# Optimization experiments

Hardware: AMD Instinct MI355X
Metric: run time of the kernel (lower is better)

Reference implementation:

```python
import jax, jax.numpy as jnp
import numpy as np

N_A = N_B = N_C = 50000
E = 800000
D_IN = 256
D_OUT = 128
T_ATT = 64


def _spmm(row, col, val, ft, n_dst):
    # sparse [n_dst, n_src] @ ft : gather src rows, scale, scatter-add to dst
    return jax.ops.segment_sum(val[:, None] * ft[col], row, num_segments=n_dst)


def setup_inputs() -> dict:
    key = jax.random.key(0)
    ks = jax.random.split(key, 40)
    f32 = jnp.float32
    inp = {
        'x_a': jax.random.normal(ks[0], (N_A, D_IN), f32),
        'x_b': jax.random.normal(ks[1], (N_B, D_IN), f32),
        'x_c': jax.random.normal(ks[2], (N_C, D_IN), f32),
    }
    # COO adjacency per relation: (dst_row, src_col, value)
    rel = {'ab': (N_A, N_B), 'ac': (N_A, N_C), 'ba': (N_B, N_A), 'ca': (N_C, N_A)}
    i = 3
    for name, (nd, ns) in rel.items():
        inp['row_' + name] = jax.random.randint(ks[i], (E,), 0, nd); i += 1
        inp['col_' + name] = jax.random.randint(ks[i], (E,), 0, ns); i += 1
        inp['val_' + name] = jax.random.uniform(ks[i], (E,), f32); i += 1
    # learned parameters (xavier-ish scale)
    def w(k, shape, s=0.05):
        return jax.random.normal(k, shape, f32) * s
    inp['w_self_a'] = w(ks[i], (D_IN, D_OUT)); i += 1
    inp['w_self_b'] = w(ks[i], (D_IN, D_OUT)); i += 1
    inp['w_self_c'] = w(ks[i], (D_IN, D_OUT)); i += 1
    inp['W_ab'] = w(ks[i], (D_IN, D_OUT)); i += 1
    inp['W_ac'] = w(ks[i], (D_IN, D_OUT)); i += 1
    inp['W_ba'] = w(ks[i], (D_IN, D_OUT)); i += 1
    inp['W_ca'] = w(ks[i], (D_IN, D_OUT)); i += 1
    inp['bias_a'] = w(ks[i], (1, D_OUT)); i += 1
    inp['bias_b'] = w(ks[i], (1, D_OUT)); i += 1
    inp['bias_c'] = w(ks[i], (1, D_OUT)); i += 1
    inp['w_cat_a'] = w(ks[i], (2 * D_OUT, D_OUT)); i += 1
    inp['w_cat_b'] = w(ks[i], (2 * D_OUT, D_OUT)); i += 1
    inp['w_cat_c'] = w(ks[i], (2 * D_OUT, D_OUT)); i += 1
    inp['w_query_a'] = w(ks[i], (D_OUT, T_ATT)); i += 1
    inp['w_keys_a'] = w(ks[i], (D_OUT, T_ATT)); i += 1
    inp['w_att_a'] = w(ks[i], (2 * T_ATT, 1)); i += 1
    return inp


def reference(x_a, x_b, x_c,
              row_ab, col_ab, val_ab, row_ac, col_ac, val_ac,
              row_ba, col_ba, val_ba, row_ca, col_ca, val_ca,
              w_self_a, w_self_b, w_self_c,
              W_ab, W_ac, W_ba, W_ca,
              bias_a, bias_b, bias_c,
              w_cat_a, w_cat_b, w_cat_c,
              w_query_a, w_keys_a, w_att_a):
    # ---- type 'a': neighbors [b, c], attention fusion ----
    self_a = x_a @ w_self_a                                   # [Na, D]
    nb_b = _spmm(row_ab, col_ab, val_ab, x_b @ W_ab, N_A)     # [Na, D]
    nb_c = _spmm(row_ac, col_ac, val_ac, x_c @ W_ac, N_A)     # [Na, D]
    q = self_a @ w_query_a                                    # [Na, T]
    e_b = jax.nn.elu(jnp.concatenate([nb_b @ w_keys_a, q], 1) @ w_att_a)  # [Na, 1]
    e_c = jax.nn.elu(jnp.concatenate([nb_c @ w_keys_a, q], 1) @ w_att_a)  # [Na, 1]
    att = jax.nn.softmax(jnp.concatenate([e_b, e_c], 1), axis=1)          # [Na, 2]
    agg_a = nb_b * att[:, :1] + nb_c * att[:, 1:2]
    out_a = jnp.concatenate([agg_a, self_a], 1) @ w_cat_a + bias_a
    # ---- type 'b': single neighbor 'a' ----
    self_b = x_b @ w_self_b
    agg_b = _spmm(row_ba, col_ba, val_ba, x_a @ W_ba, N_B)
    out_b = jnp.concatenate([agg_b, self_b], 1) @ w_cat_b + bias_b
    # ---- type 'c': single neighbor 'a' ----
    self_c = x_c @ w_self_c
    agg_c = _spmm(row_ca, col_ca, val_ca, x_a @ W_ca, N_C)
    out_c = jnp.concatenate([agg_c, self_c], 1) @ w_cat_c + bias_c
    # concat per-type outputs (all D_OUT wide) into one array
    return jnp.concatenate([out_a, out_b, out_c], 0)          # [Na+Nb+Nc, D]
```

## Files before the change

kernel.cpp:

```cpp
#include <hip/hip_runtime.h>

#define NA 50000
#define NE 800000
#define NBKT 196
#define CAP 4608
#define BSTRIDE (NBKT * CAP)

typedef unsigned int   u32;
typedef unsigned short u16;
typedef short s16x8 __attribute__((ext_vector_type(8)));
typedef float f32x4 __attribute__((ext_vector_type(4)));

__device__ __forceinline__ u16 f2bf(float f) {
  u32 u = __float_as_uint(f);
  u += 0x7fffu + ((u >> 16) & 1u);
  return (u16)(u >> 16);
}

__device__ __forceinline__ void acc8(float* a, uint4 q, float v) {
  a[0] += v * __uint_as_float(q.x << 16);
  a[1] += v * __uint_as_float(q.x & 0xffff0000u);
  a[2] += v * __uint_as_float(q.y << 16);
  a[3] += v * __uint_as_float(q.y & 0xffff0000u);
  a[4] += v * __uint_as_float(q.z << 16);
  a[5] += v * __uint_as_float(q.z & 0xffff0000u);
  a[6] += v * __uint_as_float(q.w << 16);
  a[7] += v * __uint_as_float(q.w & 0xffff0000u);
}

struct Rel4 { const int* row[4]; const int* col[4]; const float* val[4]; };

struct Prep {
  const float* src[10]; u16* dst[10];
  const float* wq; const float* wk; const float* wa; float* uvp;
  u32* gcur;
};

struct ConvArgs { const float* x[3]; u16* xb; };

struct FtArgs { const u16* A[3]; const u16* Bt[3]; u16* C[3]; };

struct FuseW { const u16* Wf[3]; const float* bias[3]; float* out[3]; };

__global__ __launch_bounds__(256) void k_prep(Prep P) {
  int gy = blockIdx.y;
  if (gy < 7) {
    int idx = blockIdx.x * 256 + threadIdx.x;
    int k = idx & 255, n = idx >> 8;
    P.dst[gy][n * 256 + k] = f2bf(P.src[gy][k * 128 + n]);
  } else if (gy < 10) {
    int idx = blockIdx.x * 256 + threadIdx.x;
    int e = idx & 7, l = (idx >> 3) & 63, jj = (idx >> 9) & 7, ks = idx >> 12;
    int n = jj * 16 + (l & 15);
    int k = ks * 32 + ((l >> 4) * 8) + e;
    P.dst[gy][idx] = f2bf(P.src[gy][k * 128 + n]);
  } else if (blockIdx.x == 0) {
    int t = threadIdx.x;
    int d = t & 127, which = t >> 7;
    const float* w = which ? P.wq : P.wk;
    const float* a = P.wa + which * 64;
    float s = 0.f;
    for (int i = 0; i < 64; ++i) s += w[d * 64 + i] * a[i];
    P.uvp[which * 128 + d] = s;
  } else if (blockIdx.x == 1) {
    for (int i = threadIdx.x; i < 1024; i += 256)
      P.gcur[i] = (u32)((i & 255) * CAP);
  }
}

__global__ __launch_bounds__(256) void k_main1(Rel4 R, u32* __restrict__ gcur,
                                               uint2* __restrict__ pairs, ConvArgs CA) {
  __shared__ __align__(16) char smem[40960];
  const int gy = blockIdx.y;
  const int t = threadIdx.x;
  if (gy < 4) {
    if (blockIdx.x >= 196) return;
    int rel = gy;
    int e0 = blockIdx.x * 4096;
    int nrem = min(4096, NE - e0);
    u32* sw0  = (u32*)smem;
    u32* sval = sw0 + 4096;
    unsigned char* sbkt = (unsigned char*)(sval + 4096);
    u32* hist  = (u32*)(sbkt + 4096);
    u32* lscan = hist + 256;
    u32* cnt2  = lscan + 256;
    u32* gbase = cnt2 + 256;
    hist[t] = 0; cnt2[t] = 0;
    __syncthreads();
    const int* rr = R.row[rel];
    const int* cc = R.col[rel];
    const float* vl = R.val[rel];
    u32 w0[16]; u32 vv[16]; int bb[16];
    #pragma unroll
    for (int i = 0; i < 16; ++i) {
      int li = t + i * 256;
      bool ok = li < nrem;
      int idx = e0 + (ok ? li : 0);
      int r = ok ? rr[idx] : 0;
      int c = ok ? cc[idx] : 0;
      float v = ok ? vl[idx] : 0.f;
      u32 b = (u32)r >> 8;
      w0[i] = (u32)(c & 0xFFFF) | ((u32)(r & 255) << 16) | (b << 24);
      vv[i] = __float_as_uint(v);
      bb[i] = ok ? (int)b : -1;
      if (ok) atomicAdd(&hist[b], 1u);
    }
    __syncthreads();
    lscan[t] = hist[t];
    __syncthreads();
    for (int ofs = 1; ofs < 256; ofs <<= 1) {
      u32 y = (t >= ofs) ? lscan[t - ofs] : 0u;
      __syncthreads();
      lscan[t] += y;
      __syncthreads();
    }
    gbase[t] = atomicAdd(&gcur[rel * 256 + t], hist[t]);
    #pragma unroll
    for (int i = 0; i < 16; ++i) {
      if (bb[i] >= 0) {
        int b = bb[i];
        u32 p = (lscan[b] - hist[b]) + atomicAdd(&cnt2[b], 1u);
        sw0[p] = w0[i]; sval[p] = vv[i]; sbkt[p] = (unsigned char)b;
      }
    }
    __syncthreads();
    uint2* P = pairs + (size_t)rel * BSTRIDE;
    #pragma unroll
    for (int i = 0; i < 16; ++i) {
      int p = t + i * 256;
      if (p < nrem) {
        int b = sbkt[p];
        u32 gd = gbase[b] + (u32)p - (lscan[b] - hist[b]);
        uint2 pr; pr.x = sw0[p]; pr.y = sval[p];
        P[gd] = pr;
      }
    }
  } else {
    const size_t TOT = 38400000;
    const size_t TSZ = 12800000;
    size_t base = ((size_t)(gy - 4) * 391 + blockIdx.x) * 16384 + (size_t)t * 8;
    #pragma unroll
    for (int it = 0; it < 8; ++it) {
      size_t g = base + (size_t)it * 2048;
      if (g < TOT) {
        int which = (g >= 2 * TSZ) ? 2 : (g >= TSZ ? 1 : 0);
        size_t off = g - (size_t)which * TSZ;
        const float* sp = CA.x[which] + off;
        float4 v0 = *(const float4*)(sp);
        float4 v1 = *(const float4*)(sp + 4);
        s16x8 o;
        o[0] = (short)f2bf(v0.x); o[1] = (short)f2bf(v0.y);
        o[2] = (short)f2bf(v0.z); o[3] = (short)f2bf(v0.w);
        o[4] = (short)f2bf(v1.x); o[5] = (short)f2bf(v1.y);
        o[6] = (short)f2bf(v1.z); o[7] = (short)f2bf(v1.w);
        *(s16x8*)(CA.xb + g) = o;
      }
    }
  }
}

__global__ __launch_bounds__(256) void k_main2(const u32* __restrict__ gcur,
    int* __restrict__ ofs_s, int* __restrict__ ofs_e,
    const uint2* __restrict__ pairs, u32* __restrict__ epak, FtArgs Ar) {
  __shared__ __align__(16) char smem[40960];
  const int gy = blockIdx.y;
  const int t = threadIdx.x;
  if (gy < 4) {
    if (blockIdx.x >= 196) return;
    int rel = gy;
    int b = blockIdx.x;
    int base = b * CAP;
    int n = (int)gcur[rel * 256 + b] - base;
    u32* sw0  = (u32*)smem;
    u32* sv   = sw0 + CAP;
    u32* hist = sv + CAP;
    u32* scan = hist + 256;
    u32* cur  = scan + 256;
    hist[t] = 0;
    __syncthreads();
    const uint2* P = pairs + (size_t)rel * BSTRIDE;
    for (int p = t; p < n; p += 256) {
      uint2 pr = P[base + p];
      sw0[p] = pr.x; sv[p] = pr.y;
      atomicAdd(&hist[(pr.x >> 16) & 255], 1u);
    }
    __syncthreads();
    u32 own = hist[t];
    scan[t] = own;
    __syncthreads();
    for (int ofs = 1; ofs < 256; ofs <<= 1) {
      u32 y = (t >= ofs) ? scan[t - ofs] : 0u;
      __syncthreads();
      scan[t] += y;
      __syncthreads();
    }
    u32 excl = scan[t] - own;
    cur[t] = excl;
    int r0 = b << 8;
    if (r0 + t < NA) {
      ofs_s[(size_t)rel * NA + r0 + t] = base + (int)excl;
      ofs_e[(size_t)rel * NA + r0 + t] = base + (int)(excl + own);
    }
    __syncthreads();
    u32* E = epak + (size_t)rel * BSTRIDE;
    for (int p = t; p < n; p += 256) {
      u32 w = sw0[p];
      int rl = (w >> 16) & 255;
      u32 d = atomicAdd(&cur[rl], 1u);
      E[base + (int)d] = (w & 0xFFFFu) | ((u32)f2bf(__uint_as_float(sv[p])) << 16);
    }
  } else {
    u16* Al = (u16*)smem;
    u16* Bl = Al + 128 * 72;
    const int by = gy - 4;
    const int which = (by < 3) ? 0 : (by < 5 ? 1 : 2);
    const int col0 = (by - (which == 0 ? 0 : (which == 1 ? 3 : 5))) * 128;
    const int ldc = (which == 0) ? 384 : 256;
    const u16* A = Ar.A[which];
    const u16* Bt = Ar.Bt[which] + (size_t)col0 * 256;
    u16* C = Ar.C[which] + col0;
    const int row0 = blockIdx.x * 128;
    const int w = t >> 6, l = t & 63;
    const int wr = (w >> 1) * 64, wc = (w & 1) * 64;
    const int sr = t >> 1, kb = (t & 1) * 32;
    f32x4 acc[4][4] = {};
    for (int kk = 0; kk < 4; ++kk) {
      if (row0 + sr < NA) {
        const u16* ap = A + (size_t)(row0 + sr) * 256 + kk * 64 + kb;
        #pragma unroll
        for (int h = 0; h < 4; ++h)
          *(s16x8*)&Al[sr * 72 + kb + h * 8] = *(const s16x8*)(ap + h * 8);
      } else {
        s16x8 z = {0,0,0,0,0,0,0,0};
        #pragma unroll
        for (int h = 0; h < 4; ++h) *(s16x8*)&Al[sr * 72 + kb + h * 8] = z;
      }
      {
        const u16* bp = Bt + (size_t)sr * 256 + kk * 64 + kb;
        #pragma unroll
        for (int h = 0; h < 4; ++h)
          *(s16x8*)&Bl[sr * 72 + kb + h * 8] = *(const s16x8*)(bp + h * 8);
      }
      __syncthreads();
      #pragma unroll
      for (int ks = 0; ks < 2; ++ks) {
        s16x8 af[4], bfr[4];
        #pragma unroll
        for (int i = 0; i < 4; ++i)
          af[i] = *(const s16x8*)&Al[(wr + i * 16 + (l & 15)) * 72 + ks * 32 + (l >> 4) * 8];
        #pragma unroll
        for (int j = 0; j < 4; ++j)
          bfr[j] = *(const s16x8*)&Bl[(wc + j * 16 + (l & 15)) * 72 + ks * 32 + (l >> 4) * 8];
        #pragma unroll
        for (int i = 0; i < 4; ++i)
          #pragma unroll
          for (int j = 0; j < 4; ++j)
            acc[i][j] = __builtin_amdgcn_mfma_f32_16x16x32_bf16(af[i], bfr[j], acc[i][j], 0, 0, 0);
      }
      __syncthreads();
    }
    #pragma unroll
    for (int i = 0; i < 4; ++i)
      #pragma unroll
      for (int j = 0; j < 4; ++j)
        #pragma unroll
        for (int q = 0; q < 4; ++q) {
          int r = row0 + wr + i * 16 + (l >> 4) * 4 + q;
          if (r < NA) C[(size_t)r * ldc + wc + j * 16 + (l & 15)] = f2bf(acc[i][j][q]);
        }
  }
}

__global__ __launch_bounds__(256) void k_spmm(
    const int* __restrict__ ofs_s, const int* __restrict__ ofs_e,
    const u32* __restrict__ epak,
    const u16* __restrict__ ya, const u16* __restrict__ yb, const u16* __restrict__ yc,
    const float* __restrict__ uv, FuseW FW) {
  __shared__ u16 Asm[16 * 264];
  int tid = threadIdx.x;
  int lane = tid & 63, wid = tid >> 6;
  int g = lane >> 4, gl = lane & 15;
  int lr = wid * 4 + g;
  int row = blockIdx.x * 16 + lr;
  int gy = blockIdx.y;
  if (gy == 0) {
    float fb[8] = {0,0,0,0,0,0,0,0};
    float fc[8] = {0,0,0,0,0,0,0,0};
    {
      const u32* pr = epak;
      int i = ofs_s[row], e = ofs_e[row];
      for (; i + 4 <= e; i += 4) {
        u32 p0 = pr[i], p1 = pr[i + 1], p2 = pr[i + 2], p3 = pr[i + 3];
        uint4 q0 = *(const uint4*)((const u32*)(yb + (size_t)(p0 & 0xFFFFu) * 256) + gl * 4);
        uint4 q1 = *(const uint4*)((const u32*)(yb + (size_t)(p1 & 0xFFFFu) * 256) + gl * 4);
        uint4 q2 = *(const uint4*)((const u32*)(yb + (size_t)(p2 & 0xFFFFu) * 256) + gl * 4);
        uint4 q3 = *(const uint4*)((const u32*)(yb + (size_t)(p3 & 0xFFFFu) * 256) + gl * 4);
        acc8(fb, q0, __uint_as_float(p0 & 0xffff0000u));
        acc8(fb, q1, __uint_as_float(p1 & 0xffff0000u));
        acc8(fb, q2, __uint_as_float(p2 & 0xffff0000u));
        acc8(fb, q3, __uint_as_float(p3 & 0xffff0000u));
      }
      for (; i < e; ++i) {
        u32 p0 = pr[i];
        uint4 q0 = *(const uint4*)((const u32*)(yb + (size_t)(p0 & 0xFFFFu) * 256) + gl * 4);
        acc8(fb, q0, __uint_as_float(p0 & 0xffff0000u));
      }
    }
    {
      const u32* pr = epak + (size_t)BSTRIDE;
      int i = ofs_s[NA + row], e = ofs_e[NA + row];
      for (; i + 4 <= e; i += 4) {
        u32 p0 = pr[i], p1 = pr[i + 1], p2 = pr[i + 2], p3 = pr[i + 3];
        uint4 q0 = *(const uint4*)((const u32*)(yc + (size_t)(p0 & 0xFFFFu) * 256) + gl * 4);
        uint4 q1 = *(const uint4*)((const u32*)(yc + (size_t)(p1 & 0xFFFFu) * 256) + gl * 4);
        uint4 q2 = *(const uint4*)((const u32*)(yc + (size_t)(p2 & 0xFFFFu) * 256) + gl * 4);
        uint4 q3 = *(const uint4*)((const u32*)(yc + (size_t)(p3 & 0xFFFFu) * 256) + gl * 4);
        acc8(fc, q0, __uint_as_float(p0 & 0xffff0000u));
        acc8(fc, q1, __uint_as_float(p1 & 0xffff0000u));
        acc8(fc, q2, __uint_as_float(p2 & 0xffff0000u));
        acc8(fc, q3, __uint_as_float(p3 & 0xffff0000u));
      }
      for (; i < e; ++i) {
        u32 p0 = pr[i];
        uint4 q0 = *(const uint4*)((const u32*)(yc + (size_t)(p0 & 0xFFFFu) * 256) + gl * 4);
        acc8(fc, q0, __uint_as_float(p0 & 0xffff0000u));
      }
    }
    uint4 sq = *(const uint4*)((const u32*)(ya + (size_t)row * 384) + gl * 4);
    float sf[8];
    sf[0] = __uint_as_float(sq.x << 16); sf[1] = __uint_as_float(sq.x & 0xffff0000u);
    sf[2] = __uint_as_float(sq.y << 16); sf[3] = __uint_as_float(sq.y & 0xffff0000u);
    sf[4] = __uint_as_float(sq.z << 16); sf[5] = __uint_as_float(sq.z & 0xffff0000u);
    sf[6] = __uint_as_float(sq.w << 16); sf[7] = __uint_as_float(sq.w & 0xffff0000u);
    float pb = 0.f, pc = 0.f, pq = 0.f;
    const float* up = uv + gl * 8;
    const float* vp = uv + 128 + gl * 8;
    #pragma unroll
    for (int j = 0; j < 8; ++j) {
      pb += fb[j] * up[j];
      pc += fc[j] * up[j];
      pq += sf[j] * vp[j];
    }
    #pragma unroll
    for (int off = 1; off < 16; off <<= 1) {
      pb += __shfl_xor(pb, off);
      pc += __shfl_xor(pc, off);
      pq += __shfl_xor(pq, off);
    }
    float eb = pb + pq, ec = pc + pq;
    eb = eb > 0.f ? eb : (expf(eb) - 1.f);
    ec = ec > 0.f ? ec : (expf(ec) - 1.f);
    float m = fmaxf(eb, ec);
    float p0 = expf(eb - m), p1 = expf(ec - m);
    float inv = 1.f / (p0 + p1);
    float a0 = p0 * inv, a1 = p1 * inv;
    s16x8 av;
    #pragma unroll
    for (int j = 0; j < 8; ++j) av[j] = (short)f2bf(a0 * fb[j] + a1 * fc[j]);
    *(s16x8*)&Asm[lr * 264 + gl * 8] = av;
    *(s16x8*)&Asm[lr * 264 + 128 + gl * 8] = *(s16x8*)&sq;
  } else {
    int which = gy - 1;
    const int* os = ofs_s + (2 + which) * NA;
    const int* oe = ofs_e + (2 + which) * NA;
    const u32* pr = epak + (size_t)(2 + which) * BSTRIDE;
    const u16* ft = ya + (which ? 256 : 128);
    const u16* selfp = which ? yc : yb;
    float fa[8] = {0,0,0,0,0,0,0,0};
    int i = os[row], e = oe[row];
    for (; i + 4 <= e; i += 4) {
      u32 p0 = pr[i], p1 = pr[i + 1], p2 = pr[i + 2], p3 = pr[i + 3];
      uint4 q0 = *(const uint4*)((const u32*)(ft + (size_t)(p0 & 0xFFFFu) * 384) + gl * 4);
      uint4 q1 = *(const uint4*)((const u32*)(ft + (size_t)(p1 & 0xFFFFu) * 384) + gl * 4);
      uint4 q2 = *(const uint4*)((const u32*)(ft + (size_t)(p2 & 0xFFFFu) * 384) + gl * 4);
      uint4 q3 = *(const uint4*)((const u32*)(ft + (size_t)(p3 & 0xFFFFu) * 384) + gl * 4);
      acc8(fa, q0, __uint_as_float(p0 & 0xffff0000u));
      acc8(fa, q1, __uint_as_float(p1 & 0xffff0000u));
      acc8(fa, q2, __uint_as_float(p2 & 0xffff0000u));
      acc8(fa, q3, __uint_as_float(p3 & 0xffff0000u));
    }
    for (; i < e; ++i) {
      u32 p0 = pr[i];
      uint4 q0 = *(const uint4*)((const u32*)(ft + (size_t)(p0 & 0xFFFFu) * 384) + gl * 4);
      acc8(fa, q0, __uint_as_float(p0 & 0xffff0000u));
    }
    s16x8 av;
    #pragma unroll
    for (int j = 0; j < 8; ++j) av[j] = (short)f2bf(fa[j]);
    *(s16x8*)&Asm[lr * 264 + gl * 8] = av;
    *(s16x8*)&Asm[lr * 264 + 128 + gl * 8] =
        *(const s16x8*)(selfp + (size_t)row * 256 + 128 + gl * 8);
  }
  __syncthreads();
  const u16* Wf = FW.Wf[gy];
  const float* bias = FW.bias[gy];
  float* outp = FW.out[gy];
  const int j0 = wid * 2, j1 = wid * 2 + 1;
  f32x4 acc0 = {0.f, 0.f, 0.f, 0.f}, acc1 = {0.f, 0.f, 0.f, 0.f};
  #pragma unroll
  for (int ks = 0; ks < 8; ++ks) {
    s16x8 a = *(const s16x8*)&Asm[(lane & 15) * 264 + ks * 32 + (lane >> 4) * 8];
    s16x8 b0 = *(const s16x8*)(Wf + ((size_t)(ks * 8 + j0) * 64 + lane) * 8);
    s16x8 b1 = *(const s16x8*)(Wf + ((size_t)(ks * 8 + j1) * 64 + lane) * 8);
    acc0 = __builtin_amdgcn_mfma_f32_16x16x32_bf16(a, b0, acc0, 0, 0, 0);
    acc1 = __builtin_amdgcn_mfma_f32_16x16x32_bf16(a, b1, acc1, 0, 0, 0);
  }
  const int c0 = j0 * 16 + (lane & 15), c1 = j1 * 16 + (lane & 15);
  const float b0v = bias[c0], b1v = bias[c1];
  const int rbase = blockIdx.x * 16 + (lane >> 4) * 4;
  #pragma unroll
  for (int q = 0; q < 4; ++q) {
    outp[(size_t)(rbase + q) * 128 + c0] = acc0[q] + b0v;
    outp[(size_t)(rbase + q) * 128 + c1] = acc1[q] + b1v;
  }
}

extern "C" void kernel_launch(void* const* d_in, const int* in_sizes, int n_in,
                              void* d_out, int out_size, void* d_ws, size_t ws_size,
                              hipStream_t stream) {
  const float* x_a = (const float*)d_in[0];
  const float* x_b = (const float*)d_in[1];
  const float* x_c = (const float*)d_in[2];
  const int* row_ab = (const int*)d_in[3];
  const int* col_ab = (const int*)d_in[4];
  const float* val_ab = (const float*)d_in[5];
  const int* row_ac = (const int*)d_in[6];
  const int* col_ac = (const int*)d_in[7];
  const float* val_ac = (const float*)d_in[8];
  const int* row_ba = (const int*)d_in[9];
  const int* col_ba = (const int*)d_in[10];
  const float* val_ba = (const float*)d_in[11];
  const int* row_ca = (const int*)d_in[12];
  const int* col_ca = (const int*)d_in[13];
  const float* val_ca = (const float*)d_in[14];
  const float* w_self_a = (const float*)d_in[15];
  const float* w_self_b = (const float*)d_in[16];
  const float* w_self_c = (const float*)d_in[17];
  const float* W_ab = (const float*)d_in[18];
  const float* W_ac = (const float*)d_in[19];
  const float* W_ba = (const float*)d_in[20];
  const float* W_ca = (const float*)d_in[21];
  const float* bias_a = (const float*)d_in[22];
  const float* bias_b = (const float*)d_in[23];
  const float* bias_c = (const float*)d_in[24];
  const float* w_cat_a = (const float*)d_in[25];
  const float* w_cat_b = (const float*)d_in[26];
  const float* w_cat_c = (const float*)d_in[27];
  const float* w_query_a = (const float*)d_in[28];
  const float* w_keys_a = (const float*)d_in[29];
  const float* w_att_a = (const float*)d_in[30];

  float* out = (float*)d_out;

  char* ws = (char*)d_ws;
  size_t off_b = 0;
  auto walloc = [&](size_t bytes) {
    void* p = ws + off_b;
    off_b = (off_b + bytes + 255) & ~(size_t)255;
    return p;
  };
  u16* ya = (u16*)walloc((size_t)NA * 384 * 2);
  u16* yb = (u16*)walloc((size_t)NA * 256 * 2);
  u16* yc = (u16*)walloc((size_t)NA * 256 * 2);
  int* ofs_s = (int*)walloc((size_t)4 * NA * 4);
  int* ofs_e = (int*)walloc((size_t)4 * NA * 4);
  u32* gcur = (u32*)walloc((size_t)4 * 256 * 4);
  uint2* pairs = (uint2*)walloc((size_t)4 * BSTRIDE * 8);
  u32* epak = (u32*)walloc((size_t)4 * BSTRIDE * 4);
  u16* Wa_t = (u16*)walloc((size_t)384 * 256 * 2);
  u16* Wb_t = (u16*)walloc((size_t)256 * 256 * 2);
  u16* Wc_t = (u16*)walloc((size_t)256 * 256 * 2);
  u16* Wcat_a = (u16*)walloc((size_t)128 * 256 * 2);
  u16* Wcat_b = (u16*)walloc((size_t)128 * 256 * 2);
  u16* Wcat_c = (u16*)walloc((size_t)128 * 256 * 2);
  float* uvbuf = (float*)walloc(256 * 4);
  u16* xb = (u16*)walloc((size_t)3 * NA * 256 * 2);

  Rel4 R;
  R.row[0] = row_ab; R.col[0] = col_ab; R.val[0] = val_ab;
  R.row[1] = row_ac; R.col[1] = col_ac; R.val[1] = val_ac;
  R.row[2] = row_ba; R.col[2] = col_ba; R.val[2] = val_ba;
  R.row[3] = row_ca; R.col[3] = col_ca; R.val[3] = val_ca;

  Prep P;
  P.src[0] = w_self_a; P.dst[0] = Wa_t;
  P.src[1] = W_ba;     P.dst[1] = Wa_t + 128 * 256;
  P.src[2] = W_ca;     P.dst[2] = Wa_t + 256 * 256;
  P.src[3] = W_ab;     P.dst[3] = Wb_t;
  P.src[4] = w_self_b; P.dst[4] = Wb_t + 128 * 256;
  P.src[5] = W_ac;     P.dst[5] = Wc_t;
  P.src[6] = w_self_c; P.dst[6] = Wc_t + 128 * 256;
  P.src[7] = w_cat_a;  P.dst[7] = Wcat_a;
  P.src[8] = w_cat_b;  P.dst[8] = Wcat_b;
  P.src[9] = w_cat_c;  P.dst[9] = Wcat_c;
  P.wq = w_query_a; P.wk = w_keys_a; P.wa = w_att_a; P.uvp = uvbuf;
  P.gcur = gcur;

  dim3 gp(128, 11);
  k_prep<<<gp, 256, 0, stream>>>(P);

  ConvArgs CA;
  CA.x[0] = x_a; CA.x[1] = x_b; CA.x[2] = x_c;
  CA.xb = xb;
  dim3 g1(391, 11);
  k_main1<<<g1, 256, 0, stream>>>(R, gcur, pairs, CA);

  FtArgs FA;
  FA.A[0] = xb; FA.A[1] = xb + (size_t)NA * 256; FA.A[2] = xb + (size_t)2 * NA * 256;
  FA.Bt[0] = Wa_t; FA.Bt[1] = Wb_t; FA.Bt[2] = Wc_t;
  FA.C[0] = ya; FA.C[1] = yb; FA.C[2] = yc;
  dim3 g2(391, 11);
  k_main2<<<g2, 256, 0, stream>>>(gcur, ofs_s, ofs_e, pairs, epak, FA);

  FuseW FW;
  FW.Wf[0] = Wcat_a; FW.Wf[1] = Wcat_b; FW.Wf[2] = Wcat_c;
  FW.bias[0] = bias_a; FW.bias[1] = bias_b; FW.bias[2] = bias_c;
  FW.out[0] = out; FW.out[1] = out + (size_t)NA * 128; FW.out[2] = out + (size_t)NA * 128 * 2;
  dim3 gs(3125, 3);
  k_spmm<<<gs, 256, 0, stream>>>(ofs_s, ofs_e, epak, ya, yb, yc, uvbuf, FW);
}
```

Before: 279.3 us.

## Split each row's edge list across four lane groups per wave with shuffle reduction

```diff
diff --git a/kernel.cpp b/kernel.cpp
--- a/kernel.cpp
+++ b/kernel.cpp
@@ -280,116 +280,128 @@
   int tid = threadIdx.x;
   int lane = tid & 63, wid = tid >> 6;
   int g = lane >> 4, gl = lane & 15;
-  int lr = wid * 4 + g;
-  int row = blockIdx.x * 16 + lr;
+  const u32 glb = (u32)gl * 16;
   int gy = blockIdx.y;
   if (gy == 0) {
-    float fb[8] = {0,0,0,0,0,0,0,0};
-    float fc[8] = {0,0,0,0,0,0,0,0};
-    {
-      const u32* pr = epak;
-      int i = ofs_s[row], e = ofs_e[row];
-      for (; i + 4 <= e; i += 4) {
-        u32 p0 = pr[i], p1 = pr[i + 1], p2 = pr[i + 2], p3 = pr[i + 3];
-        uint4 q0 = *(const uint4*)((const u32*)(yb + (size_t)(p0 & 0xFFFFu) * 256) + gl * 4);
-        uint4 q1 = *(const uint4*)((const u32*)(yb + (size_t)(p1 & 0xFFFFu) * 256) + gl * 4);
-        uint4 q2 = *(const uint4*)((const u32*)(yb + (size_t)(p2 & 0xFFFFu) * 256) + gl * 4);
-        uint4 q3 = *(const uint4*)((const u32*)(yb + (size_t)(p3 & 0xFFFFu) * 256) + gl * 4);
-        acc8(fb, q0, __uint_as_float(p0 & 0xffff0000u));
-        acc8(fb, q1, __uint_as_float(p1 & 0xffff0000u));
-        acc8(fb, q2, __uint_as_float(p2 & 0xffff0000u));
-        acc8(fb, q3, __uint_as_float(p3 & 0xffff0000u));
-      }
-      for (; i < e; ++i) {
-        u32 p0 = pr[i];
-        uint4 q0 = *(const uint4*)((const u32*)(yb + (size_t)(p0 & 0xFFFFu) * 256) + gl * 4);
-        acc8(fb, q0, __uint_as_float(p0 & 0xffff0000u));
-      }
-    }
-    {
-      const u32* pr = epak + (size_t)BSTRIDE;
-      int i = ofs_s[NA + row], e = ofs_e[NA + row];
-      for (; i + 4 <= e; i += 4) {
-        u32 p0 = pr[i], p1 = pr[i + 1], p2 = pr[i + 2], p3 = pr[i + 3];
-        uint4 q0 = *(const uint4*)((const u32*)(yc + (size_t)(p0 & 0xFFFFu) * 256) + gl * 4);
-        uint4 q1 = *(const uint4*)((const u32*)(yc + (size_t)(p1 & 0xFFFFu) * 256) + gl * 4);
-        uint4 q2 = *(const uint4*)((const u32*)(yc + (size_t)(p2 & 0xFFFFu) * 256) + gl * 4);
-        uint4 q3 = *(const uint4*)((const u32*)(yc + (size_t)(p3 & 0xFFFFu) * 256) + gl * 4);
-        acc8(fc, q0, __uint_as_float(p0 & 0xffff0000u));
-        acc8(fc, q1, __uint_as_float(p1 & 0xffff0000u));
-        acc8(fc, q2, __uint_as_float(p2 & 0xffff0000u));
-        acc8(fc, q3, __uint_as_float(p3 & 0xffff0000u));
-      }
-      for (; i < e; ++i) {
-        u32 p0 = pr[i];
-        uint4 q0 = *(const uint4*)((const u32*)(yc + (size_t)(p0 & 0xFFFFu) * 256) + gl * 4);
-        acc8(fc, q0, __uint_as_float(p0 & 0xffff0000u));
-      }
-    }
-    uint4 sq = *(const uint4*)((const u32*)(ya + (size_t)row * 384) + gl * 4);
-    float sf[8];
-    sf[0] = __uint_as_float(sq.x << 16); sf[1] = __uint_as_float(sq.x & 0xffff0000u);
-    sf[2] = __uint_as_float(sq.y << 16); sf[3] = __uint_as_float(sq.y & 0xffff0000u);
-    sf[4] = __uint_as_float(sq.z << 16); sf[5] = __uint_as_float(sq.z & 0xffff0000u);
-    sf[6] = __uint_as_float(sq.w << 16); sf[7] = __uint_as_float(sq.w & 0xffff0000u);
-    float pb = 0.f, pc = 0.f, pq = 0.f;
-    const float* up = uv + gl * 8;
-    const float* vp = uv + 128 + gl * 8;
-    #pragma unroll
-    for (int j = 0; j < 8; ++j) {
-      pb += fb[j] * up[j];
-      pc += fc[j] * up[j];
-      pq += sf[j] * vp[j];
-    }
-    #pragma unroll
-    for (int off = 1; off < 16; off <<= 1) {
-      pb += __shfl_xor(pb, off);
-      pc += __shfl_xor(pc, off);
-      pq += __shfl_xor(pq, off);
-    }
-    float eb = pb + pq, ec = pc + pq;
-    eb = eb > 0.f ? eb : (expf(eb) - 1.f);
-    ec = ec > 0.f ? ec : (expf(ec) - 1.f);
-    float m = fmaxf(eb, ec);
-    float p0 = expf(eb - m), p1 = expf(ec - m);
-    float inv = 1.f / (p0 + p1);
-    float a0 = p0 * inv, a1 = p1 * inv;
-    s16x8 av;
-    #pragma unroll
-    for (int j = 0; j < 8; ++j) av[j] = (short)f2bf(a0 * fb[j] + a1 * fc[j]);
-    *(s16x8*)&Asm[lr * 264 + gl * 8] = av;
-    *(s16x8*)&Asm[lr * 264 + 128 + gl * 8] = *(s16x8*)&sq;
+    const char* ybase = (const char*)yb;
+    const char* cbase = (const char*)yc;
+    for (int rr = 0; rr < 4; ++rr) {
+      const int lr = wid * 4 + rr;
+      const int row = blockIdx.x * 16 + lr;
+      float fb[8] = {0,0,0,0,0,0,0,0};
+      float fc[8] = {0,0,0,0,0,0,0,0};
+      {
+        int e = ofs_e[row];
+        int i = ofs_s[row] + g;
+        for (; i + 4 < e; i += 8) {
+          u32 p0 = epak[i], p1 = epak[i + 4];
+          uint4 q0 = *(const uint4*)(ybase + (((p0 & 0xFFFFu) << 9) + glb));
+          uint4 q1 = *(const uint4*)(ybase + (((p1 & 0xFFFFu) << 9) + glb));
+          acc8(fb, q0, __uint_as_float(p0 & 0xffff0000u));
+          acc8(fb, q1, __uint_as_float(p1 & 0xffff0000u));
+        }
+        if (i < e) {
+          u32 p0 = epak[i];
+          uint4 q0 = *(const uint4*)(ybase + (((p0 & 0xFFFFu) << 9) + glb));
+          acc8(fb, q0, __uint_as_float(p0 & 0xffff0000u));
+        }
+      }
+      {
+        const u32* pr = epak + BSTRIDE;
+        int e = ofs_e[NA + row];
+        int i = ofs_s[NA + row] + g;
+        for (; i + 4 < e; i += 8) {
+          u32 p0 = pr[i], p1 = pr[i + 4];
+          uint4 q0 = *(const uint4*)(cbase + (((p0 & 0xFFFFu) << 9) + glb));
+          uint4 q1 = *(const uint4*)(cbase + (((p1 & 0xFFFFu) << 9) + glb));
+          acc8(fc, q0, __uint_as_float(p0 & 0xffff0000u));
+          acc8(fc, q1, __uint_as_float(p1 & 0xffff0000u));
+        }
+        if (i < e) {
+          u32 p0 = pr[i];
+          uint4 q0 = *(const uint4*)(cbase + (((p0 & 0xFFFFu) << 9) + glb));
+          acc8(fc, q0, __uint_as_float(p0 & 0xffff0000u));
+        }
+      }
+      #pragma unroll
+      for (int j = 0; j < 8; ++j) {
+        fb[j] += __shfl_xor(fb[j], 16); fb[j] += __shfl_xor(fb[j], 32);
+        fc[j] += __shfl_xor(fc[j], 16); fc[j] += __shfl_xor(fc[j], 32);
+      }
+      if (g == 0) {
+        uint4 sq = *(const uint4*)((const char*)ya + (u32)row * 768 + glb);
+        float sf[8];
+        sf[0] = __uint_as_float(sq.x << 16); sf[1] = __uint_as_float(sq.x & 0xffff0000u);
+        sf[2] = __uint_as_float(sq.y << 16); sf[3] = __uint_as_float(sq.y & 0xffff0000u);
+        sf[4] = __uint_as_float(sq.z << 16); sf[5] = __uint_as_float(sq.z & 0xffff0000u);
+        sf[6] = __uint_as_float(sq.w << 16); sf[7] = __uint_as_float(sq.w & 0xffff0000u);
+        float pb = 0.f, pc = 0.f, pq = 0.f;
+        const float* up = uv + gl * 8;
+        const float* vp = uv + 128 + gl * 8;
+        #pragma unroll
+        for (int j = 0; j < 8; ++j) {
+          pb += fb[j] * up[j];
+          pc += fc[j] * up[j];
+          pq += sf[j] * vp[j];
+        }
+        #pragma unroll
+        for (int off = 1; off < 16; off <<= 1) {
+          pb += __shfl_xor(pb, off);
+          pc += __shfl_xor(pc, off);
+          pq += __shfl_xor(pq, off);
+        }
+        float eb = pb + pq, ec = pc + pq;
+        eb = eb > 0.f ? eb : (expf(eb) - 1.f);
+        ec = ec > 0.f ? ec : (expf(ec) - 1.f);
+        float m = fmaxf(eb, ec);
+        float p0 = expf(eb - m), p1 = expf(ec - m);
+        float inv = 1.f / (p0 + p1);
+        float a0 = p0 * inv, a1 = p1 * inv;
+        s16x8 av;
+        #pragma unroll
+        for (int j = 0; j < 8; ++j) av[j] = (short)f2bf(a0 * fb[j] + a1 * fc[j]);
+        *(s16x8*)&Asm[lr * 264 + gl * 8] = av;
+        *(s16x8*)&Asm[lr * 264 + 128 + gl * 8] = *(s16x8*)&sq;
+      }
+    }
   } else {
-    int which = gy - 1;
+    const int which = gy - 1;
     const int* os = ofs_s + (2 + which) * NA;
     const int* oe = ofs_e + (2 + which) * NA;
     const u32* pr = epak + (size_t)(2 + which) * BSTRIDE;
-    const u16* ft = ya + (which ? 256 : 128);
-    const u16* selfp = which ? yc : yb;
-    float fa[8] = {0,0,0,0,0,0,0,0};
-    int i = os[row], e = oe[row];
-    for (; i + 4 <= e; i += 4) {
-      u32 p0 = pr[i], p1 = pr[i + 1], p2 = pr[i + 2], p3 = pr[i + 3];
-      uint4 q0 = *(const uint4*)((const u32*)(ft + (size_t)(p0 & 0xFFFFu) * 384) + gl * 4);
-      uint4 q1 = *(const uint4*)((const u32*)(ft + (size_t)(p1 & 0xFFFFu) * 384) + gl * 4);
-      uint4 q2 = *(const uint4*)((const u32*)(ft + (size_t)(p2 & 0xFFFFu) * 384) + gl * 4);
-      uint4 q3 = *(const uint4*)((const u32*)(ft + (size_t)(p3 & 0xFFFFu) * 384) + gl * 4);
-      acc8(fa, q0, __uint_as_float(p0 & 0xffff0000u));
-      acc8(fa, q1, __uint_as_float(p1 & 0xffff0000u));
-      acc8(fa, q2, __uint_as_float(p2 & 0xffff0000u));
-      acc8(fa, q3, __uint_as_float(p3 & 0xffff0000u));
-    }
-    for (; i < e; ++i) {
-      u32 p0 = pr[i];
-      uint4 q0 = *(const uint4*)((const u32*)(ft + (size_t)(p0 & 0xFFFFu) * 384) + gl * 4);
-      acc8(fa, q0, __uint_as_float(p0 & 0xffff0000u));
-    }
-    s16x8 av;
-    #pragma unroll
-    for (int j = 0; j < 8; ++j) av[j] = (short)f2bf(fa[j]);
-    *(s16x8*)&Asm[lr * 264 + gl * 8] = av;
-    *(s16x8*)&Asm[lr * 264 + 128 + gl * 8] =
-        *(const s16x8*)(selfp + (size_t)row * 256 + 128 + gl * 8);
+    const char* fbase = (const char*)ya + (which ? 512 : 256);
+    const char* selfp = (const char*)(which ? yc : yb);
+    for (int rr = 0; rr < 4; ++rr) {
+      const int lr = wid * 4 + rr;
+      const int row = blockIdx.x * 16 + lr;
+      float fa[8] = {0,0,0,0,0,0,0,0};
+      int e = oe[row];
+      int i = os[row] + g;
+      for (; i + 4 < e; i += 8) {
+        u32 p0 = pr[i], p1 = pr[i + 4];
+        uint4 q0 = *(const uint4*)(fbase + ((p0 & 0xFFFFu) * 768u + glb));
+        uint4 q1 = *(const uint4*)(fbase + ((p1 & 0xFFFFu) * 768u + glb));
+        acc8(fa, q0, __uint_as_float(p0 & 0xffff0000u));
+        acc8(fa, q1, __uint_as_float(p1 & 0xffff0000u));
+      }
+      if (i < e) {
+        u32 p0 = pr[i];
+        uint4 q0 = *(const uint4*)(fbase + ((p0 & 0xFFFFu) * 768u + glb));
+        acc8(fa, q0, __uint_as_float(p0 & 0xffff0000u));
+      }
+      #pragma unroll
+      for (int j = 0; j < 8; ++j) {
+        fa[j] += __shfl_xor(fa[j], 16); fa[j] += __shfl_xor(fa[j], 32);
+      }
+      if (g == 0) {
+        s16x8 av;
+        #pragma unroll
+        for (int j = 0; j < 8; ++j) av[j] = (short)f2bf(fa[j]);
+        *(s16x8*)&Asm[lr * 264 + gl * 8] = av;
+        *(s16x8*)&Asm[lr * 264 + 128 + gl * 8] =
+            *(const s16x8*)(selfp + (u32)row * 512 + 256 + glb);
+      }
+    }
   }
   __syncthreads();
   const u16* Wf = FW.Wf[gy];
```

Result: slower. 336.6 us (+20.5%).
